# Optimization experiments

Hardware: AMD Instinct MI355X
Metric: run time of the kernel (lower is better)

Reference implementation:

```python
import jax, jax.numpy as jnp
import numpy as np

B = 16
PATCH_NUM = 32      # L of inter branch
PATCH_SIZE = 128    # L of intra branch
WIN_SIZE = PATCH_NUM * PATCH_SIZE  # 4096
H = 8
E = 64


def setup_inputs() -> dict:
    key = jax.random.key(0)
    ks = jax.random.split(key, 6)
    return {
        "q_inter": jax.random.normal(ks[0], (B, PATCH_NUM, H, E), jnp.float32),
        "k_inter": jax.random.normal(ks[1], (B, PATCH_NUM, H, E), jnp.float32),
        "v_inter": jax.random.normal(ks[2], (B, PATCH_NUM, H, E), jnp.float32),
        "q_intra": jax.random.normal(ks[3], (B, PATCH_SIZE, H, E), jnp.float32),
        "k_intra": jax.random.normal(ks[4], (B, PATCH_SIZE, H, E), jnp.float32),
        "v_intra": jax.random.normal(ks[5], (B, PATCH_SIZE, H, E), jnp.float32),
    }


def _full_attention(q, k, v):
    # q,k,v: [B, L, H, E]; full softmax attention, scale = 1/sqrt(E)
    scale = 1.0 / jnp.sqrt(jnp.asarray(q.shape[-1], q.dtype))
    score = jnp.einsum('blhe,bshe->bhls', q, k) * scale
    att = jax.nn.softmax(score, axis=-1)  # dropout is identity in eval mode
    return jnp.einsum('bhls,bshd->blhd', att, v)


def reference(q_inter, k_inter, v_inter, q_intra, k_intra, v_intra):
    V_inter = _full_attention(q_inter, k_inter, v_inter)  # [B, patch_num, H, E]
    V_intra = _full_attention(q_intra, k_intra, v_intra)  # [B, patch_size, H, E]
    # einops repeat 'b pn h d -> b (pn ps) h d': each patch repeated ps times
    V_inter_up = jnp.repeat(V_inter, PATCH_SIZE, axis=1)  # [B, win_size, H, E]
    # einops repeat 'b ps h d -> b (ps pn) h d': each position repeated pn times
    V_intra_up = jnp.repeat(V_intra, PATCH_NUM, axis=1)   # [B, win_size, H, E]
    return V_inter_up + V_intra_up
```

## Files before the change

### kernel.cpp

```cpp
#include <hip/hip_runtime.h>


#define NH 8
#define NE 64
#define ROWSTRIDE (NH * NE)

typedef float vf4 __attribute__((ext_vector_type(4)));

__device__ __forceinline__ float dot4(const float4 a, const float4 b) {
    return a.x * b.x + a.y * b.y + a.z * b.z + a.w * b.w;
}

template <int L>
__device__ __forceinline__ void attn_block(
    const int bid, const float* __restrict__ qg_, const float* __restrict__ kg_,
    const float* __restrict__ vg_, float* __restrict__ dst,
    float* sKs, float* sVs, float* sQs)
{
    constexpr int TILES = L / 32;
    constexpr int CPT   = L / 32;
    constexpr int SST   = L + 4;
    constexpr int KST   = 68;
    constexpr int QST   = 68;
    constexpr int VST   = 64;

    const int tid  = threadIdx.x;
    const int tile = bid % TILES;
    const int h    = (bid / TILES) % NH;
    const int b    = bid / (TILES * NH);
    const int r0   = tile * 32;

    const float* kg = kg_ + ((size_t)b * L * NH + h) * NE;
    const float* vg = vg_ + ((size_t)b * L * NH + h) * NE;
    const float* qg = qg_ + ((size_t)(b * L + r0) * NH + h) * NE;

    for (int idx = tid; idx < L * 16; idx += 256) {
        const int row = idx >> 4;
        const int f   = (idx & 15) * 4;
        *(float4*)&sKs[row * KST + f] = *(const float4*)(kg + (size_t)row * ROWSTRIDE + f);
        *(float4*)&sVs[row * VST + f] = *(const float4*)(vg + (size_t)row * ROWSTRIDE + f);
    }
    for (int idx = tid; idx < 32 * 16; idx += 256) {
        const int row = idx >> 4;
        const int f   = (idx & 15) * 4;
        *(float4*)&sQs[row * QST + f] = *(const float4*)(qg + (size_t)row * ROWSTRIDE + f);
    }
    __syncthreads();

    const int rg = tid >> 5;
    const int cg = tid & 31;
    const int rr = rg * 4;
    float acc[4][CPT];
    #pragma unroll
    for (int i = 0; i < 4; i++)
        #pragma unroll
        for (int j = 0; j < CPT; j++) acc[i][j] = 0.f;

    #pragma unroll
    for (int e = 0; e < NE; e += 4) {
        float4 qv[4], kv[CPT];
        #pragma unroll
        for (int i = 0; i < 4; i++) qv[i] = *(const float4*)&sQs[(rr + i) * QST + e];
        #pragma unroll
        for (int j = 0; j < CPT; j++) kv[j] = *(const float4*)&sKs[(cg + j * 32) * KST + e];
        #pragma unroll
        for (int i = 0; i < 4; i++)
            #pragma unroll
            for (int j = 0; j < CPT; j++)
                acc[i][j] += dot4(qv[i], kv[j]);
    }
    __syncthreads();

    float* S = sKs;

    #pragma unroll
    for (int i = 0; i < 4; i++) {
        float m = acc[i][0] * 0.125f;
        #pragma unroll
        for (int j = 1; j < CPT; j++) m = fmaxf(m, acc[i][j] * 0.125f);
        #pragma unroll
        for (int msk = 1; msk < 32; msk <<= 1) m = fmaxf(m, __shfl_xor(m, msk));
        float p[CPT], s = 0.f;
        #pragma unroll
        for (int j = 0; j < CPT; j++) { p[j] = __expf(acc[i][j] * 0.125f - m); s += p[j]; }
        #pragma unroll
        for (int msk = 1; msk < 32; msk <<= 1) s += __shfl_xor(s, msk);
        const float inv = 1.f / s;
        #pragma unroll
        for (int j = 0; j < CPT; j++)
            S[(rr + i) * SST + cg + 32 * j] = p[j] * inv;
    }
    __syncthreads();

    const int r   = tid >> 3;
    const int sub = tid & 7;
    const int e0  = sub * 8;
    float a0=0,a1=0,a2=0,a3=0,a4=0,a5=0,a6=0,a7=0;
    for (int c0 = 0; c0 < L; c0 += 4) {
        const float4 p4 = *(const float4*)&S[r * SST + c0];
        const float pv[4] = { p4.x, p4.y, p4.z, p4.w };
        #pragma unroll
        for (int u = 0; u < 4; u++) {
            const float p  = pv[u];
            const float4 va = *(const float4*)&sVs[(c0 + u) * VST + e0];
            const float4 vb = *(const float4*)&sVs[(c0 + u) * VST + e0 + 4];
            a0 += p * va.x; a1 += p * va.y; a2 += p * va.z; a3 += p * va.w;
            a4 += p * vb.x; a5 += p * vb.y; a6 += p * vb.z; a7 += p * vb.w;
        }
    }
    float* w = dst + ((size_t)(b * L + r0 + r) * NH + h) * NE + e0;
    *(float4*)w       = make_float4(a0, a1, a2, a3);
    *(float4*)(w + 4) = make_float4(a4, a5, a6, a7);
}

__global__ __launch_bounds__(256, 2) void attn_fused(
    const float* __restrict__ qI, const float* __restrict__ kI, const float* __restrict__ vI,
    const float* __restrict__ qT, const float* __restrict__ kT, const float* __restrict__ vT,
    float* __restrict__ wsI, float* __restrict__ wsT)
{
    __shared__ __align__(16) float sKs[128 * 68];
    __shared__ __align__(16) float sVs[128 * 64];
    __shared__ __align__(16) float sQs[32 * 68];

    const int bid = blockIdx.x;
    const int grp = bid / 5;
    const int rem = bid - grp * 5;
    if (rem < 4)
        attn_block<128>(grp * 4 + rem, qT, kT, vT, wsT, sKs, sVs, sQs);
    else
        attn_block<32>(grp, qI, kI, vI, wsI, sKs, sVs, sQs);
}

__global__ __launch_bounds__(256) void upsample_add_kernel(
    const float4* __restrict__ wsI, const float4* __restrict__ wsT,
    float* __restrict__ out)
{
    const int t  = blockIdx.x * 256 + threadIdx.x;
    const int e4 = t & 15;
    const int h  = (t >> 4) & 7;
    const int g  = (t >> 7) & 3;
    const int pn = (t >> 9) & 31;
    const int b  = t >> 14;

    const float4 a = wsI[((b * 32 + pn) * NH + h) * 16 + e4];
    const float4 c = wsT[((b * 128 + pn * 4 + g) * NH + h) * 16 + e4];
    vf4 s;
    s.x = a.x + c.x; s.y = a.y + c.y; s.z = a.z + c.z; s.w = a.w + c.w;

    float* o = out + ((((size_t)b * 4096 + pn * 128 + g * 32) * NH + h) * 16 + e4) * 4;
    #pragma unroll
    for (int j = 0; j < 32; j++)
        __builtin_nontemporal_store(s, (vf4*)(o + (size_t)j * ROWSTRIDE));
}

extern "C" void kernel_launch(void* const* d_in, const int* in_sizes, int n_in,
                              void* d_out, int out_size, void* d_ws, size_t ws_size,
                              hipStream_t stream) {
    const float* q_inter = (const float*)d_in[0];
    const float* k_inter = (const float*)d_in[1];
    const float* v_inter = (const float*)d_in[2];
    const float* q_intra = (const float*)d_in[3];
    const float* k_intra = (const float*)d_in[4];
    const float* v_intra = (const float*)d_in[5];
    float* out = (float*)d_out;
    float* wsI = (float*)d_ws;
    float* wsT = wsI + (size_t)16 * 32 * NH * NE;

    attn_fused<<<640, 256, 0, stream>>>(
        q_inter, k_inter, v_inter, q_intra, k_intra, v_intra, wsI, wsT);

    upsample_add_kernel<<<1024, 256, 0, stream>>>(
        (const float4*)wsI, (const float4*)wsT, out);
}
```

Measured before the change: 184.0 us.

## Fuse inter/intra attention and upsample-add into a single kernel

Merges the two attention branches and the repeat-and-add upsampling into one kernel with 512 blocks. Each block first computes 8 inter-branch rows with one warp per row and keeps them in shared memory. It then computes its 32-row intra-branch tile and writes the summed result, repeated 32 times, straight to the output with nontemporal stores. This removes the second launch and the workspace write and read-back. In exchange, the large output write now runs at the end of each attention block instead of in a separate high-parallelism kernel, which lowers grid size and the overlap between compute and stores.

```diff
diff --git a/kernel.cpp b/kernel.cpp
--- a/kernel.cpp
+++ b/kernel.cpp
@@ -11,62 +11,113 @@
     return a.x * b.x + a.y * b.y + a.z * b.z + a.w * b.w;
 }
 
-template <int L>
-__device__ __forceinline__ void attn_block(
-    const int bid, const float* __restrict__ qg_, const float* __restrict__ kg_,
-    const float* __restrict__ vg_, float* __restrict__ dst,
-    float* sKs, float* sVs, float* sQs)
+__global__ __launch_bounds__(256, 2) void temp_attn_mega(
+    const float* __restrict__ qI, const float* __restrict__ kI, const float* __restrict__ vI,
+    const float* __restrict__ qT, const float* __restrict__ kT, const float* __restrict__ vT,
+    float* __restrict__ out)
 {
-    constexpr int TILES = L / 32;
-    constexpr int CPT   = L / 32;
-    constexpr int SST   = L + 4;
-    constexpr int KST   = 68;
-    constexpr int QST   = 68;
-    constexpr int VST   = 64;
+    __shared__ __align__(16) float sKs[128 * 68];
+    __shared__ __align__(16) float sVs[128 * 64];
+    __shared__ __align__(16) float sQs[32 * 68];
+    __shared__ __align__(16) float sIO[8 * 68];
 
     const int tid  = threadIdx.x;
-    const int tile = bid % TILES;
-    const int h    = (bid / TILES) % NH;
-    const int b    = bid / (TILES * NH);
+    const int bid  = blockIdx.x;
+    const int tile = bid & 3;
+    const int h    = (bid >> 2) & 7;
+    const int b    = bid >> 5;
     const int r0   = tile * 32;
+    const int pn0  = tile * 8;
 
-    const float* kg = kg_ + ((size_t)b * L * NH + h) * NE;
-    const float* vg = vg_ + ((size_t)b * L * NH + h) * NE;
-    const float* qg = qg_ + ((size_t)(b * L + r0) * NH + h) * NE;
+    {
+        const float* kg = kI + ((size_t)b * 32 * NH + h) * NE;
+        const float* vg = vI + ((size_t)b * 32 * NH + h) * NE;
+        float* dK = sKs;
+        float* dV = sKs + 32 * 68;
+        for (int idx = tid; idx < 32 * 16; idx += 256) {
+            const int row = idx >> 4;
+            const int f   = (idx & 15) * 4;
+            *(float4*)&dK[row * 68 + f] = *(const float4*)(kg + (size_t)row * ROWSTRIDE + f);
+            *(float4*)&dV[row * 64 + f] = *(const float4*)(vg + (size_t)row * ROWSTRIDE + f);
+        }
+    }
+    __syncthreads();
+    {
+        const int rg = tid >> 5;
+        const int ln = tid & 31;
+        const float* dK = sKs;
+        const float* dV = sKs + 32 * 68;
 
-    for (int idx = tid; idx < L * 16; idx += 256) {
-        const int row = idx >> 4;
-        const int f   = (idx & 15) * 4;
-        *(float4*)&sKs[row * KST + f] = *(const float4*)(kg + (size_t)row * ROWSTRIDE + f);
-        *(float4*)&sVs[row * VST + f] = *(const float4*)(vg + (size_t)row * ROWSTRIDE + f);
+        const float* qrow = qI + ((size_t)(b * 32 + pn0 + rg) * NH + h) * NE;
+        float s = 0.f;
+        #pragma unroll
+        for (int e = 0; e < NE; e += 4) {
+            const float4 qv = *(const float4*)(qrow + e);
+            const float4 kv = *(const float4*)&dK[ln * 68 + e];
+            s += dot4(qv, kv);
+        }
+        s *= 0.125f;
+        float m = s;
+        #pragma unroll
+        for (int msk = 1; msk < 32; msk <<= 1) m = fmaxf(m, __shfl_xor(m, msk));
+        const float p = __expf(s - m);
+        float sum = p;
+        #pragma unroll
+        for (int msk = 1; msk < 32; msk <<= 1) sum += __shfl_xor(sum, msk);
+        const float pn = p / sum;
+
+        const int hw = tid & 32;
+        float o0 = 0.f, o1 = 0.f;
+        #pragma unroll 8
+        for (int c = 0; c < 32; c++) {
+            const float pc = __shfl(pn, hw + c);
+            const float2 v = *(const float2*)&dV[c * 64 + ln * 2];
+            o0 += pc * v.x;
+            o1 += pc * v.y;
+        }
+        sIO[rg * 68 + ln * 2]     = o0;
+        sIO[rg * 68 + ln * 2 + 1] = o1;
     }
-    for (int idx = tid; idx < 32 * 16; idx += 256) {
-        const int row = idx >> 4;
-        const int f   = (idx & 15) * 4;
-        *(float4*)&sQs[row * QST + f] = *(const float4*)(qg + (size_t)row * ROWSTRIDE + f);
+    __syncthreads();
+
+    {
+        const float* kg = kT + ((size_t)b * 128 * NH + h) * NE;
+        const float* vg = vT + ((size_t)b * 128 * NH + h) * NE;
+        const float* qg = qT + ((size_t)(b * 128 + r0) * NH + h) * NE;
+        for (int idx = tid; idx < 128 * 16; idx += 256) {
+            const int row = idx >> 4;
+            const int f   = (idx & 15) * 4;
+            *(float4*)&sKs[row * 68 + f] = *(const float4*)(kg + (size_t)row * ROWSTRIDE + f);
+            *(float4*)&sVs[row * 64 + f] = *(const float4*)(vg + (size_t)row * ROWSTRIDE + f);
+        }
+        for (int idx = tid; idx < 32 * 16; idx += 256) {
+            const int row = idx >> 4;
+            const int f   = (idx & 15) * 4;
+            *(float4*)&sQs[row * 68 + f] = *(const float4*)(qg + (size_t)row * ROWSTRIDE + f);
+        }
     }
     __syncthreads();
 
     const int rg = tid >> 5;
     const int cg = tid & 31;
     const int rr = rg * 4;
-    float acc[4][CPT];
+    float acc[4][4];
     #pragma unroll
     for (int i = 0; i < 4; i++)
         #pragma unroll
-        for (int j = 0; j < CPT; j++) acc[i][j] = 0.f;
+        for (int j = 0; j < 4; j++) acc[i][j] = 0.f;
 
     #pragma unroll
     for (int e = 0; e < NE; e += 4) {
-        float4 qv[4], kv[CPT];
+        float4 qv[4], kv[4];
         #pragma unroll
-        for (int i = 0; i < 4; i++) qv[i] = *(const float4*)&sQs[(rr + i) * QST + e];
+        for (int i = 0; i < 4; i++) qv[i] = *(const float4*)&sQs[(rr + i) * 68 + e];
         #pragma unroll
-        for (int j = 0; j < CPT; j++) kv[j] = *(const float4*)&sKs[(cg + j * 32) * KST + e];
+        for (int j = 0; j < 4; j++) kv[j] = *(const float4*)&sKs[(cg + j * 32) * 68 + e];
         #pragma unroll
         for (int i = 0; i < 4; i++)
             #pragma unroll
-            for (int j = 0; j < CPT; j++)
+            for (int j = 0; j < 4; j++)
                 acc[i][j] += dot4(qv[i], kv[j]);
     }
     __syncthreads();
@@ -77,18 +128,18 @@
     for (int i = 0; i < 4; i++) {
         float m = acc[i][0] * 0.125f;
         #pragma unroll
-        for (int j = 1; j < CPT; j++) m = fmaxf(m, acc[i][j] * 0.125f);
+        for (int j = 1; j < 4; j++) m = fmaxf(m, acc[i][j] * 0.125f);
         #pragma unroll
         for (int msk = 1; msk < 32; msk <<= 1) m = fmaxf(m, __shfl_xor(m, msk));
-        float p[CPT], s = 0.f;
+        float p[4], s = 0.f;
         #pragma unroll
-        for (int j = 0; j < CPT; j++) { p[j] = __expf(acc[i][j] * 0.125f - m); s += p[j]; }
+        for (int j = 0; j < 4; j++) { p[j] = __expf(acc[i][j] * 0.125f - m); s += p[j]; }
         #pragma unroll
         for (int msk = 1; msk < 32; msk <<= 1) s += __shfl_xor(s, msk);
         const float inv = 1.f / s;
         #pragma unroll
-        for (int j = 0; j < CPT; j++)
-            S[(rr + i) * SST + cg + 32 * j] = p[j] * inv;
+        for (int j = 0; j < 4; j++)
+            S[(rr + i) * 132 + cg + 32 * j] = p[j] * inv;
     }
     __syncthreads();
 
@@ -96,61 +147,33 @@
     const int sub = tid & 7;
     const int e0  = sub * 8;
     float a0=0,a1=0,a2=0,a3=0,a4=0,a5=0,a6=0,a7=0;
-    for (int c0 = 0; c0 < L; c0 += 4) {
-        const float4 p4 = *(const float4*)&S[r * SST + c0];
+    for (int c0 = 0; c0 < 128; c0 += 4) {
+        const float4 p4 = *(const float4*)&S[r * 132 + c0];
         const float pv[4] = { p4.x, p4.y, p4.z, p4.w };
         #pragma unroll
         for (int u = 0; u < 4; u++) {
             const float p  = pv[u];
-            const float4 va = *(const float4*)&sVs[(c0 + u) * VST + e0];
-            const float4 vb = *(const float4*)&sVs[(c0 + u) * VST + e0 + 4];
+            const float4 va = *(const float4*)&sVs[(c0 + u) * 64 + e0];
+            const float4 vb = *(const float4*)&sVs[(c0 + u) * 64 + e0 + 4];
             a0 += p * va.x; a1 += p * va.y; a2 += p * va.z; a3 += p * va.w;
             a4 += p * vb.x; a5 += p * vb.y; a6 += p * vb.z; a7 += p * vb.w;
         }
     }
-    float* w = dst + ((size_t)(b * L + r0 + r) * NH + h) * NE + e0;
-    *(float4*)w       = make_float4(a0, a1, a2, a3);
-    *(float4*)(w + 4) = make_float4(a4, a5, a6, a7);
-}
 
-__global__ __launch_bounds__(256, 2) void attn_fused(
-    const float* __restrict__ qI, const float* __restrict__ kI, const float* __restrict__ vI,
-    const float* __restrict__ qT, const float* __restrict__ kT, const float* __restrict__ vT,
-    float* __restrict__ wsI, float* __restrict__ wsT)
-{
-    __shared__ __align__(16) float sKs[128 * 68];
-    __shared__ __align__(16) float sVs[128 * 64];
-    __shared__ __align__(16) float sQs[32 * 68];
+    const int io = (r >> 2) * 68 + e0;
+    const float4 iA = *(const float4*)&sIO[io];
+    const float4 iB = *(const float4*)&sIO[io + 4];
+    vf4 oA, oB;
+    oA.x = a0 + iA.x; oA.y = a1 + iA.y; oA.z = a2 + iA.z; oA.w = a3 + iA.w;
+    oB.x = a4 + iB.x; oB.y = a5 + iB.y; oB.z = a6 + iB.z; oB.w = a7 + iB.w;
 
-    const int bid = blockIdx.x;
-    const int grp = bid / 5;
-    const int rem = bid - grp * 5;
-    if (rem < 4)
-        attn_block<128>(grp * 4 + rem, qT, kT, vT, wsT, sKs, sVs, sQs);
-    else
-        attn_block<32>(grp, qI, kI, vI, wsI, sKs, sVs, sQs);
-}
-
-__global__ __launch_bounds__(256) void upsample_add_kernel(
-    const float4* __restrict__ wsI, const float4* __restrict__ wsT,
-    float* __restrict__ out)
-{
-    const int t  = blockIdx.x * 256 + threadIdx.x;
-    const int e4 = t & 15;
-    const int h  = (t >> 4) & 7;
-    const int g  = (t >> 7) & 3;
-    const int pn = (t >> 9) & 31;
-    const int b  = t >> 14;
-
-    const float4 a = wsI[((b * 32 + pn) * NH + h) * 16 + e4];
-    const float4 c = wsT[((b * 128 + pn * 4 + g) * NH + h) * 16 + e4];
-    vf4 s;
-    s.x = a.x + c.x; s.y = a.y + c.y; s.z = a.z + c.z; s.w = a.w + c.w;
-
-    float* o = out + ((((size_t)b * 4096 + pn * 128 + g * 32) * NH + h) * 16 + e4) * 4;
+    const int i = r0 + r;
+    float* ob = out + ((size_t)(b * 4096 + i * 32) * NH + h) * NE + e0;
     #pragma unroll
-    for (int j = 0; j < 32; j++)
-        __builtin_nontemporal_store(s, (vf4*)(o + (size_t)j * ROWSTRIDE));
+    for (int j = 0; j < 32; j++) {
+        __builtin_nontemporal_store(oA, (vf4*)(ob + (size_t)j * ROWSTRIDE));
+        __builtin_nontemporal_store(oB, (vf4*)(ob + (size_t)j * ROWSTRIDE + 4));
+    }
 }
 
 extern "C" void kernel_launch(void* const* d_in, const int* in_sizes, int n_in,
@@ -163,12 +186,8 @@
     const float* k_intra = (const float*)d_in[4];
     const float* v_intra = (const float*)d_in[5];
     float* out = (float*)d_out;
-    float* wsI = (float*)d_ws;
-    float* wsT = wsI + (size_t)16 * 32 * NH * NE;
+    (void)d_ws; (void)ws_size;
 
-    attn_fused<<<640, 256, 0, stream>>>(
-        q_inter, k_inter, v_inter, q_intra, k_intra, v_intra, wsI, wsT);
-
-    upsample_add_kernel<<<1024, 256, 0, stream>>>(
-        (const float4*)wsI, (const float4*)wsT, out);
+    temp_attn_mega<<<512, 256, 0, stream>>>(
+        q_inter, k_inter, v_inter, q_intra, k_intra, v_intra, out);
 }
```

New measurement: 205.2 us. 11.5% more time.
